# Performance work log

Measured on AMD Instinct MI355X. Metric: run time of the kernel, lower is better.

The kernel has to match this reference:

```python
import jax, jax.numpy as jnp
import numpy as np

K = 32               # number of instance labels (reduce_max(labels)+1, fixed for jit)
PUSH_MARGIN = 0.25
PULL_MARGIN = 0.0
PUSH_WEIGHT = 1.0
PULL_WEIGHT = 1.0
REG_WEIGHT = 1e-4


def setup_inputs() -> dict:
    key = jax.random.key(0)
    k1, k2 = jax.random.split(key)
    embeddings = jax.random.normal(k1, (8, 512, 512, 16), dtype=jnp.float32)
    labels = jax.random.randint(k2, (8, 512, 512), 0, K, dtype=jnp.int32)
    return {"embeddings": embeddings, "labels": labels}


def _per_image_loss(emb, lab):
    # emb: [H,W,C] -> [N,C]; lab: [H,W] -> [N]
    C = emb.shape[-1]
    emb = emb.reshape(-1, C)
    lab = lab.reshape(-1)

    # compute_centroids: single-pass segment mean (replaces O(n*k) masked loop)
    counts = jax.ops.segment_sum(jnp.ones_like(lab, dtype=jnp.float32), lab, num_segments=K)  # [K]
    sums = jax.ops.segment_sum(emb, lab, num_segments=K)                                      # [K,C]
    valid = counts > 0                                                                        # [K]
    centroids = jnp.where(valid[:, None], sums / jnp.maximum(counts, 1.0)[:, None], 0.0)
    nv = jnp.sum(valid.astype(jnp.float32))

    # push loss: pairwise Manhattan distances between valid centroids, strictly upper triangle
    pdist = jnp.sum(jnp.abs(centroids[:, None, :] - centroids[None, :, :]), axis=-1)  # [K,K]
    hinge = jax.nn.relu(PUSH_MARGIN - pdist)
    pair_mask = (valid[:, None] & valid[None, :]) & jnp.triu(jnp.ones((K, K), bool), 1)
    ncomp = nv * (nv - 1.0) / 2.0
    push = jnp.where(
        nv >= 2.0,
        jnp.sum(jnp.square(hinge) * pair_mask) / jnp.maximum(ncomp, 1.0),
        0.0,
    )

    # pull loss: Manhattan distance of each point to its own centroid, squared-error, mean
    own = centroids[lab]                                   # [N,C] gather
    d = jnp.sum(jnp.abs(emb - own), axis=-1)               # [N]
    pull = jnp.mean(jnp.square(jax.nn.relu(d - PULL_MARGIN)))

    # regularization: mean of squared entries of VALID centroids
    reg = jnp.sum(jnp.square(centroids) * valid[:, None]) / jnp.maximum(nv * C, 1.0)

    return PUSH_WEIGHT * push + PULL_WEIGHT * pull + REG_WEIGHT * reg


def reference(embeddings, labels):
    per_image = jax.vmap(_per_image_loss)(embeddings, labels)  # [B]
    return jnp.mean(per_image)
```

## Files before the change

kernel.cpp:

```cpp
#include <hip/hip_runtime.h>

#define KC 32
#define CH 16
#define NB 8
#define NPI (512*512)

#define SBPI 256
#define SPPB (NPI/SBPI)
#define SPW  (SPPB/4)
#define SCH  (SPW/64)

#define PBPI 256
#define PPPB (NPI/PBPI)
#define PIT  (PPPB/256)

#define WS_PART 0
#define WS_SUMS (WS_PART + NB*SBPI*544)
#define WS_CEN (WS_SUMS + NB*544)
#define WS_PR  (WS_CEN + NB*CH*KC)
#define WS_PLP (WS_PR + NB)

typedef float f32x16 __attribute__((ext_vector_type(16)));
typedef short short8 __attribute__((ext_vector_type(8)));

__device__ __forceinline__ unsigned short f2bf(float x) {
  unsigned u = __builtin_bit_cast(unsigned, x);
  u += 0x7FFFu + ((u >> 16) & 1u);
  return (unsigned short)(u >> 16);
}
__device__ __forceinline__ unsigned packbf(float lo, float hi) {
  return (unsigned)f2bf(lo) | ((unsigned)f2bf(hi) << 16);
}

__global__ __launch_bounds__(256) void segsum_kernel(
    const float4* __restrict__ embv, const int* __restrict__ lab,
    float* __restrict__ ws) {
  __shared__ unsigned smem[4][8][68];
  __shared__ int      slab[4][64];
  __shared__ float    sred[4][KC * 17];

  const int t = threadIdx.x, w = t >> 6, l = t & 63;
  const int b = blockIdx.x / SBPI, blk = blockIdx.x % SBPI;
  const size_t base = (size_t)b * NPI + (size_t)blk * SPPB + (size_t)w * SPW;
  const int h = l >> 5;
  const int m = l & 31;

  f32x16 acc;
  #pragma unroll
  for (int i = 0; i < 16; ++i) acc[i] = 0.f;

  float4 c0, c1, c2, c3; int cl;
  {
    const float4* ep = embv + (base + l) * 4;
    c0 = ep[0]; c1 = ep[1]; c2 = ep[2]; c3 = ep[3];
    cl = lab[base + l];
  }

  for (int ch = 0; ch < SCH; ++ch) {
    smem[w][0][l] = packbf(c0.x, c0.y);
    smem[w][1][l] = packbf(c0.z, c0.w);
    smem[w][2][l] = packbf(c1.x, c1.y);
    smem[w][3][l] = packbf(c1.z, c1.w);
    smem[w][4][l] = packbf(c2.x, c2.y);
    smem[w][5][l] = packbf(c2.z, c2.w);
    smem[w][6][l] = packbf(c3.x, c3.y);
    smem[w][7][l] = packbf(c3.z, c3.w);
    slab[w][l] = cl;

    if (ch + 1 < SCH) {
      const size_t p = base + (size_t)(ch + 1) * 64 + l;
      const float4* ep = embv + p * 4;
      c0 = ep[0]; c1 = ep[1]; c2 = ep[2]; c3 = ep[3];
      cl = lab[p];
    }

    #pragma unroll
    for (int s = 0; s < 4; ++s) {
      const int4* lp = (const int4*)&slab[w][s * 16 + 8 * h];
      const int4 la = lp[0], lb = lp[1];
      const short ONE = (short)0x3F80;
      short8 av;
      av[0] = (la.x == m) ? ONE : (short)0; av[1] = (la.y == m) ? ONE : (short)0;
      av[2] = (la.z == m) ? ONE : (short)0; av[3] = (la.w == m) ? ONE : (short)0;
      av[4] = (lb.x == m) ? ONE : (short)0; av[5] = (lb.y == m) ? ONE : (short)0;
      av[6] = (lb.z == m) ? ONE : (short)0; av[7] = (lb.w == m) ? ONE : (short)0;

      short8 bv;
      if (m < CH) {
        const uint4* fp = (const uint4*)&smem[w][m >> 1][s * 16 + 8 * h];
        const uint4 u0 = fp[0], u1 = fp[1];
        const unsigned sh = (unsigned)(m & 1) * 16u;
        bv[0] = (short)((u0.x >> sh) & 0xFFFFu); bv[1] = (short)((u0.y >> sh) & 0xFFFFu);
        bv[2] = (short)((u0.z >> sh) & 0xFFFFu); bv[3] = (short)((u0.w >> sh) & 0xFFFFu);
        bv[4] = (short)((u1.x >> sh) & 0xFFFFu); bv[5] = (short)((u1.y >> sh) & 0xFFFFu);
        bv[6] = (short)((u1.z >> sh) & 0xFFFFu); bv[7] = (short)((u1.w >> sh) & 0xFFFFu);
      } else {
        const short cv = (m == CH) ? ONE : (short)0;
        #pragma unroll
        for (int e = 0; e < 8; ++e) bv[e] = cv;
      }
      acc = __builtin_amdgcn_mfma_f32_32x32x16_bf16(av, bv, acc, 0, 0, 0);
    }
  }

  if (m < 17) {
    #pragma unroll
    for (int r = 0; r < 16; ++r) {
      const int row = (r & 3) + 8 * (r >> 2) + 4 * h;
      sred[w][row * 17 + m] = acc[r];
    }
  }
  __syncthreads();
  for (int i = t; i < KC * 17; i += 256) {
    const float v = sred[0][i] + sred[1][i] + sred[2][i] + sred[3][i];
    ws[WS_PART + (size_t)blockIdx.x * 544 + i] = v;
  }
}

__global__ __launch_bounds__(256) void mid_reduce_kernel(float* __restrict__ ws) {
  __shared__ float part[8][33];
  const int g = blockIdx.x, t = threadIdx.x;
  const int img = g / 17, c0 = (g % 17) * 32;
  const int cidx = t & 31, ps = t >> 5;

  const float* base = ws + WS_PART + (size_t)(img * SBPI) * 544 + c0 + cidx;
  float s = 0.f;
  #pragma unroll 8
  for (int q = 0; q < SBPI / 8; ++q)
    s += base[(size_t)(ps + 8 * q) * 544];
  part[ps][cidx] = s;
  __syncthreads();
  if (t < 32) {
    float v = 0.f;
    #pragma unroll
    for (int i = 0; i < 8; ++i) v += part[i][t];
    ws[WS_SUMS + img * 544 + c0 + t] = v;
  }
}

__global__ __launch_bounds__(512) void centroid_push_kernel(float* __restrict__ ws) {
  __shared__ float sums_s[KC * 17];
  __shared__ float cent[CH * KC];
  __shared__ float validf[KC];
  __shared__ float red[8];
  const int b = blockIdx.x, t = threadIdx.x;

  for (int i = t; i < KC * 17; i += 512) sums_s[i] = ws[WS_SUMS + b * 544 + i];
  __syncthreads();

  if (t < KC) validf[t] = (sums_s[t * 17 + 16] > 0.f) ? 1.f : 0.f;

  const int k = t & 31, c = t >> 5;
  const float cnt = sums_s[k * 17 + 16];
  const float ce  = (cnt > 0.f) ? sums_s[k * 17 + c] / cnt : 0.f;
  cent[c * KC + k] = ce;
  ws[WS_CEN + (size_t)b * CH * KC + c * KC + k] = ce;
  const float regacc = ce * ce;
  __syncthreads();

  float pushacc = 0.f;
  for (int p = t; p < KC * KC; p += 512) {
    const int i = p >> 5, j = p & 31;
    if (i < j && validf[i] > 0.f && validf[j] > 0.f) {
      float pd = 0.f;
      #pragma unroll
      for (int cc = 0; cc < CH; ++cc)
        pd += fabsf(cent[cc * KC + i] - cent[cc * KC + j]);
      const float hi = 0.25f - pd;
      if (hi > 0.f) pushacc += hi * hi;
    }
  }

  float v = pushacc;
  #pragma unroll
  for (int off = 32; off; off >>= 1) v += __shfl_down(v, off, 64);
  if ((t & 63) == 0) red[t >> 6] = v;
  __syncthreads();
  float pushsum = 0.f;
  if (t == 0) { for (int i = 0; i < 8; ++i) pushsum += red[i]; }
  __syncthreads();

  v = regacc;
  #pragma unroll
  for (int off = 32; off; off >>= 1) v += __shfl_down(v, off, 64);
  if ((t & 63) == 0) red[t >> 6] = v;
  __syncthreads();

  if (t == 0) {
    float regsum = 0.f;
    for (int i = 0; i < 8; ++i) regsum += red[i];
    float nv = 0.f;
    for (int i = 0; i < KC; ++i) nv += validf[i];
    const float ncomp = nv * (nv - 1.f) * 0.5f;
    const float push  = (nv >= 2.f) ? pushsum / fmaxf(ncomp, 1.f) : 0.f;
    const float reg   = regsum / fmaxf(nv * (float)CH, 1.f);
    ws[WS_PR + b] = push + 1e-4f * reg;
  }
}

__global__ __launch_bounds__(256) void pull_kernel(
    const float4* __restrict__ embv, const int* __restrict__ lab,
    float* __restrict__ ws) {
  __shared__ float cent[CH * KC];
  __shared__ float red[4];
  const int t = threadIdx.x;
  const int b = blockIdx.x / PBPI, blk = blockIdx.x % PBPI;
  for (int i = t; i < CH * KC; i += 256)
    cent[i] = ws[WS_CEN + (size_t)b * CH * KC + i];
  __syncthreads();

  float acc = 0.f;
  const size_t pix0 = (size_t)b * NPI + (size_t)blk * PPPB;
  for (int it = 0; it < PIT; ++it) {
    const size_t p = pix0 + (size_t)it * 256 + t;
    const int L = lab[p];
    const float4 v0 = embv[p * 4 + 0];
    const float4 v1 = embv[p * 4 + 1];
    const float4 v2 = embv[p * 4 + 2];
    const float4 v3 = embv[p * 4 + 3];
    float d = 0.f;
    d += fabsf(v0.x - cent[ 0 * KC + L]);
    d += fabsf(v0.y - cent[ 1 * KC + L]);
    d += fabsf(v0.z - cent[ 2 * KC + L]);
    d += fabsf(v0.w - cent[ 3 * KC + L]);
    d += fabsf(v1.x - cent[ 4 * KC + L]);
    d += fabsf(v1.y - cent[ 5 * KC + L]);
    d += fabsf(v1.z - cent[ 6 * KC + L]);
    d += fabsf(v1.w - cent[ 7 * KC + L]);
    d += fabsf(v2.x - cent[ 8 * KC + L]);
    d += fabsf(v2.y - cent[ 9 * KC + L]);
    d += fabsf(v2.z - cent[10 * KC + L]);
    d += fabsf(v2.w - cent[11 * KC + L]);
    d += fabsf(v3.x - cent[12 * KC + L]);
    d += fabsf(v3.y - cent[13 * KC + L]);
    d += fabsf(v3.z - cent[14 * KC + L]);
    d += fabsf(v3.w - cent[15 * KC + L]);
    acc += d * d;
  }
  #pragma unroll
  for (int off = 32; off; off >>= 1) acc += __shfl_down(acc, off, 64);
  if ((t & 63) == 0) red[t >> 6] = acc;
  __syncthreads();
  if (t == 0) ws[WS_PLP + blockIdx.x] = red[0] + red[1] + red[2] + red[3];
}

__global__ void final_kernel(const float* __restrict__ ws, float* __restrict__ out) {
  __shared__ float simg[NB];
  const int t = threadIdx.x;
  const int img = t >> 5, j = t & 31;
  float v = 0.f;
  #pragma unroll
  for (int q = 0; q < PBPI / 32; ++q)
    v += ws[WS_PLP + img * PBPI + j + 32 * q];
  #pragma unroll
  for (int off = 16; off; off >>= 1) v += __shfl_down(v, off, 32);
  if (j == 0) simg[img] = v;
  __syncthreads();
  if (t == 0) {
    float s = 0.f;
    for (int b2 = 0; b2 < NB; ++b2)
      s += ws[WS_PR + b2] + simg[b2] * (1.f / (float)NPI);
    out[0] = s * (1.f / (float)NB);
  }
}

extern "C" void kernel_launch(void* const* d_in, const int* in_sizes, int n_in,
                              void* d_out, int out_size, void* d_ws, size_t ws_size,
                              hipStream_t stream) {
  const float4* emb = (const float4*)d_in[0];
  const int*    lab = (const int*)d_in[1];
  float* ws  = (float*)d_ws;
  float* out = (float*)d_out;

  hipLaunchKernelGGL(segsum_kernel, dim3(NB * SBPI), dim3(256), 0, stream, emb, lab, ws);
  hipLaunchKernelGGL(mid_reduce_kernel, dim3(NB * 17), dim3(256), 0, stream, ws);
  hipLaunchKernelGGL(centroid_push_kernel, dim3(NB), dim3(512), 0, stream, ws);
  hipLaunchKernelGGL(pull_kernel, dim3(NB * PBPI), dim3(256), 0, stream, emb, lab, ws);
  hipLaunchKernelGGL(final_kernel, dim3(1), dim3(256), 0, stream, ws, out);
}
```

Before: 58.27 us.

## Replace 32x32 MFMA segment-sum with two 16x16x32 MFMAs and integer counts

The segment-sum kernel switches from one 32x32x16 bf16 MFMA per 16 pixels, where half the output columns were padding or a count column, to two 16x16x32 MFMAs covering labels 0-15 and 16-31 with exactly 16 channel columns. Counts are now computed with integer compares and wave shuffles instead of a ones column in the matrix. The bf16 conversion uses the hardware v_cvt_pk_bf16_f32 instruction in place of manual rounding, and the LDS row padding changes to 69. The aim is to cut wasted MFMA work and VALU conversion cost, in exchange for extra compare/add VALU work for the counts.

```diff
diff --git a/kernel.cpp b/kernel.cpp
--- a/kernel.cpp
+++ b/kernel.cpp
@@ -9,6 +9,7 @@
 #define SPPB (NPI/SBPI)
 #define SPW  (SPPB/4)
 #define SCH  (SPW/64)
+#define PAD  69
 
 #define PBPI 256
 #define PPPB (NPI/PBPI)
@@ -20,34 +21,33 @@
 #define WS_PR  (WS_CEN + NB*CH*KC)
 #define WS_PLP (WS_PR + NB)
 
-typedef float f32x16 __attribute__((ext_vector_type(16)));
+typedef float f32x4 __attribute__((ext_vector_type(4)));
 typedef short short8 __attribute__((ext_vector_type(8)));
 
-__device__ __forceinline__ unsigned short f2bf(float x) {
-  unsigned u = __builtin_bit_cast(unsigned, x);
-  u += 0x7FFFu + ((u >> 16) & 1u);
-  return (unsigned short)(u >> 16);
-}
 __device__ __forceinline__ unsigned packbf(float lo, float hi) {
-  return (unsigned)f2bf(lo) | ((unsigned)f2bf(hi) << 16);
+  unsigned r;
+  asm("v_cvt_pk_bf16_f32 %0, %1, %2" : "=v"(r) : "v"(lo), "v"(hi));
+  return r;
 }
 
 __global__ __launch_bounds__(256) void segsum_kernel(
     const float4* __restrict__ embv, const int* __restrict__ lab,
     float* __restrict__ ws) {
-  __shared__ unsigned smem[4][8][68];
+  __shared__ unsigned smem[4][8][PAD];
   __shared__ int      slab[4][64];
   __shared__ float    sred[4][KC * 17];
 
   const int t = threadIdx.x, w = t >> 6, l = t & 63;
   const int b = blockIdx.x / SBPI, blk = blockIdx.x % SBPI;
   const size_t base = (size_t)b * NPI + (size_t)blk * SPPB + (size_t)w * SPW;
-  const int h = l >> 5;
-  const int m = l & 31;
-
-  f32x16 acc;
-  #pragma unroll
-  for (int i = 0; i < 16; ++i) acc[i] = 0.f;
+  const int ch = l & 15;
+  const int g  = l >> 4;
+  const int ch16 = ch + 16;
+
+  f32x4 acc0, acc1;
+  #pragma unroll
+  for (int i = 0; i < 4; ++i) { acc0[i] = 0.f; acc1[i] = 0.f; }
+  int cnt0 = 0, cnt1 = 0;
 
   float4 c0, c1, c2, c3; int cl;
   {
@@ -56,7 +56,7 @@
     cl = lab[base + l];
   }
 
-  for (int ch = 0; ch < SCH; ++ch) {
+  for (int chk = 0; chk < SCH; ++chk) {
     smem[w][0][l] = packbf(c0.x, c0.y);
     smem[w][1][l] = packbf(c0.z, c0.w);
     smem[w][2][l] = packbf(c1.x, c1.y);
@@ -67,48 +67,58 @@
     smem[w][7][l] = packbf(c3.z, c3.w);
     slab[w][l] = cl;
 
-    if (ch + 1 < SCH) {
-      const size_t p = base + (size_t)(ch + 1) * 64 + l;
+    if (chk + 1 < SCH) {
+      const size_t p = base + (size_t)(chk + 1) * 64 + l;
       const float4* ep = embv + p * 4;
       c0 = ep[0]; c1 = ep[1]; c2 = ep[2]; c3 = ep[3];
       cl = lab[p];
     }
 
     #pragma unroll
-    for (int s = 0; s < 4; ++s) {
-      const int4* lp = (const int4*)&slab[w][s * 16 + 8 * h];
-      const int4 la = lp[0], lb = lp[1];
+    for (int s = 0; s < 2; ++s) {
+      const int px0 = s * 32 + g * 8;
+      const int4 la = *(const int4*)&slab[w][px0];
+      const int4 lb = *(const int4*)&slab[w][px0 + 4];
       const short ONE = (short)0x3F80;
-      short8 av;
-      av[0] = (la.x == m) ? ONE : (short)0; av[1] = (la.y == m) ? ONE : (short)0;
-      av[2] = (la.z == m) ? ONE : (short)0; av[3] = (la.w == m) ? ONE : (short)0;
-      av[4] = (lb.x == m) ? ONE : (short)0; av[5] = (lb.y == m) ? ONE : (short)0;
-      av[6] = (lb.z == m) ? ONE : (short)0; av[7] = (lb.w == m) ? ONE : (short)0;
-
+
+      short8 a0, a1;
+      a0[0] = (la.x == ch) ? ONE : (short)0; a0[1] = (la.y == ch) ? ONE : (short)0;
+      a0[2] = (la.z == ch) ? ONE : (short)0; a0[3] = (la.w == ch) ? ONE : (short)0;
+      a0[4] = (lb.x == ch) ? ONE : (short)0; a0[5] = (lb.y == ch) ? ONE : (short)0;
+      a0[6] = (lb.z == ch) ? ONE : (short)0; a0[7] = (lb.w == ch) ? ONE : (short)0;
+      a1[0] = (la.x == ch16) ? ONE : (short)0; a1[1] = (la.y == ch16) ? ONE : (short)0;
+      a1[2] = (la.z == ch16) ? ONE : (short)0; a1[3] = (la.w == ch16) ? ONE : (short)0;
+      a1[4] = (lb.x == ch16) ? ONE : (short)0; a1[5] = (lb.y == ch16) ? ONE : (short)0;
+      a1[6] = (lb.z == ch16) ? ONE : (short)0; a1[7] = (lb.w == ch16) ? ONE : (short)0;
+      cnt0 += (la.x == ch) + (la.y == ch) + (la.z == ch) + (la.w == ch)
+            + (lb.x == ch) + (lb.y == ch) + (lb.z == ch) + (lb.w == ch);
+      cnt1 += (la.x == ch16) + (la.y == ch16) + (la.z == ch16) + (la.w == ch16)
+            + (lb.x == ch16) + (lb.y == ch16) + (lb.z == ch16) + (lb.w == ch16);
+
+      const uint4 u0 = *(const uint4*)&smem[w][ch >> 1][px0];
+      const uint4 u1 = *(const uint4*)&smem[w][ch >> 1][px0 + 4];
+      const unsigned sh = (unsigned)(ch & 1) * 16u;
       short8 bv;
-      if (m < CH) {
-        const uint4* fp = (const uint4*)&smem[w][m >> 1][s * 16 + 8 * h];
-        const uint4 u0 = fp[0], u1 = fp[1];
-        const unsigned sh = (unsigned)(m & 1) * 16u;
-        bv[0] = (short)((u0.x >> sh) & 0xFFFFu); bv[1] = (short)((u0.y >> sh) & 0xFFFFu);
-        bv[2] = (short)((u0.z >> sh) & 0xFFFFu); bv[3] = (short)((u0.w >> sh) & 0xFFFFu);
-        bv[4] = (short)((u1.x >> sh) & 0xFFFFu); bv[5] = (short)((u1.y >> sh) & 0xFFFFu);
-        bv[6] = (short)((u1.z >> sh) & 0xFFFFu); bv[7] = (short)((u1.w >> sh) & 0xFFFFu);
-      } else {
-        const short cv = (m == CH) ? ONE : (short)0;
-        #pragma unroll
-        for (int e = 0; e < 8; ++e) bv[e] = cv;
-      }
-      acc = __builtin_amdgcn_mfma_f32_32x32x16_bf16(av, bv, acc, 0, 0, 0);
+      bv[0] = (short)(u0.x >> sh); bv[1] = (short)(u0.y >> sh);
+      bv[2] = (short)(u0.z >> sh); bv[3] = (short)(u0.w >> sh);
+      bv[4] = (short)(u1.x >> sh); bv[5] = (short)(u1.y >> sh);
+      bv[6] = (short)(u1.z >> sh); bv[7] = (short)(u1.w >> sh);
+
+      acc0 = __builtin_amdgcn_mfma_f32_16x16x32_bf16(a0, bv, acc0, 0, 0, 0);
+      acc1 = __builtin_amdgcn_mfma_f32_16x16x32_bf16(a1, bv, acc1, 0, 0, 0);
     }
   }
 
-  if (m < 17) {
-    #pragma unroll
-    for (int r = 0; r < 16; ++r) {
-      const int row = (r & 3) + 8 * (r >> 2) + 4 * h;
-      sred[w][row * 17 + m] = acc[r];
-    }
+  #pragma unroll
+  for (int r = 0; r < 4; ++r) {
+    sred[w][(g * 4 + r) * 17 + ch]        = acc0[r];
+    sred[w][(g * 4 + r + 16) * 17 + ch]   = acc1[r];
+  }
+  cnt0 += __shfl_xor(cnt0, 16, 64); cnt0 += __shfl_xor(cnt0, 32, 64);
+  cnt1 += __shfl_xor(cnt1, 16, 64); cnt1 += __shfl_xor(cnt1, 32, 64);
+  if (l < 16) {
+    sred[w][l * 17 + 16]        = (float)cnt0;
+    sred[w][(l + 16) * 17 + 16] = (float)cnt1;
   }
   __syncthreads();
   for (int i = t; i < KC * 17; i += 256) {
```

Measured after the change: 58.83 us. Within noise of the previous version (+1.0%).
